# Kernel tuning notes

Hardware: AMD Instinct MI355X
Metric: run time of the kernel (lower is better)

Reference implementation:

```python
import jax, jax.numpy as jnp
import numpy as np

S, B, NIN = 64, 64, 64          # att_width (= target_seq_len), batch, num_input
H1, HB, H = 128, 128, 128       # first LSTM size, biLSTM hidden, att_hid
MLP = (1024, 512, 256, 128, 1)  # h1..h4, num_output


def _lstm_cell(x, h, c, Wih, Whh, b):
    # PyTorch gate order: i, f, g, o
    z = x @ Wih.T + h @ Whh.T + b
    i, f, g, o = jnp.split(z, 4, axis=-1)
    c = jax.nn.sigmoid(f) * c + jax.nn.sigmoid(i) * jnp.tanh(g)
    h = jax.nn.sigmoid(o) * jnp.tanh(c)
    return h, c


def _lstm_seq(xs, Wih, Whh, b, reverse=False):
    # xs: [S, B, in] -> hs: [S, B, H], final (h, c)
    h0 = jnp.zeros((xs.shape[1], Whh.shape[1]), xs.dtype)

    def step(carry, x):
        h, c = _lstm_cell(x, carry[0], carry[1], Wih, Whh, b)
        return (h, c), h

    (h, c), hs = jax.lax.scan(step, (h0, h0), xs, reverse=reverse)
    return hs, (h, c)


def _forward(input_seqs,
             lstm1_Wih, lstm1_Whh, lstm1_b,
             bi2f_Wih, bi2f_Whh, bi2f_b, bi2b_Wih, bi2b_Whh, bi2b_b,
             bi3f_Wih, bi3f_Whh, bi3f_b, bi3b_Wih, bi3b_Whh, bi3b_b,
             enc_Wih, enc_Whh, enc_b,
             dec_Wih, dec_Whh, dec_b,
             att_fc_W, att_w,
             W1_W, W1_b, W2_W, W2_b, W3_W, W3_b, W4_W, W4_b, out_W, out_b):
    # 1) one-directional LSTM
    x, _ = _lstm_seq(input_seqs, lstm1_Wih, lstm1_Whh, lstm1_b)
    # 2-3) two stacked bidirectional LSTMs
    f, _ = _lstm_seq(x, bi2f_Wih, bi2f_Whh, bi2f_b)
    bk, _ = _lstm_seq(x, bi2b_Wih, bi2b_Whh, bi2b_b, reverse=True)
    x = jnp.concatenate([f, bk], axis=-1)            # [S,B,2*HB]
    f, _ = _lstm_seq(x, bi3f_Wih, bi3f_Whh, bi3f_b)
    bk, _ = _lstm_seq(x, bi3b_Wih, bi3b_Whh, bi3b_b, reverse=True)
    x = jnp.concatenate([f, bk], axis=-1)            # [S,B,2*HB]
    # 4) encoder LSTM
    enc_out, (eh, ec) = _lstm_seq(x, enc_Wih, enc_Whh, enc_b)  # [S,B,H]
    # per-step attention decode loop (S sequential steps)
    def dec_step(carry, _):
        xin, h, c = carry
        h, c = _lstm_cell(xin, h, c, dec_Wih, dec_Whh, dec_b)   # [B,H]
        # 'concat' attention: tanh(fc(h + enc_out)) @ w -> scores over S
        scores = jnp.tanh((h[None, :, :] + enc_out) @ att_fc_W.T) @ att_w  # [S,B]
        aw = jax.nn.softmax(scores, axis=0)
        ctx = jnp.einsum('sb,sbh->bh', aw, enc_out)             # [B,H]
        out = jnp.concatenate([h, ctx], axis=-1)                # [B,2H]
        return (h, h, c), out

    _, dec_outs = jax.lax.scan(dec_step, (enc_out[-1], eh, ec), None, length=S)
    # [S,B,2H] -> [B, S*2H]
    flat = dec_outs.transpose(1, 0, 2).reshape(dec_outs.shape[1], -1)
    # 5-6) flatten + 4-layer tanh MLP + linear head
    x = jnp.tanh(flat @ W1_W.T + W1_b)
    x = jnp.tanh(x @ W2_W.T + W2_b)
    x = jnp.tanh(x @ W3_W.T + W3_b)
    x = jnp.tanh(x @ W4_W.T + W4_b)
    return x @ out_W.T + out_b


def setup_inputs() -> dict:
    key = jax.random.key(0)
    ks = iter(jax.random.split(key, 40))

    def mat(shape, scale=0.08):
        return (jax.random.normal(next(ks), shape) * scale).astype(jnp.float32)

    d = {}
    d['input_seqs'] = jax.random.normal(next(ks), (S, B, NIN), dtype=jnp.float32)

    def lstm_p(pfx, inp, hid):
        d[pfx + '_Wih'] = mat((4 * hid, inp))
        d[pfx + '_Whh'] = mat((4 * hid, hid))
        d[pfx + '_b'] = mat((4 * hid,))

    lstm_p('lstm1', NIN, H1)
    lstm_p('bi2f', H1, HB); lstm_p('bi2b', H1, HB)
    lstm_p('bi3f', 2 * HB, HB); lstm_p('bi3b', 2 * HB, HB)
    lstm_p('enc', 2 * HB, H)
    lstm_p('dec', H, H)
    d['att_fc_W'] = mat((H, H))
    d['att_w'] = mat((H,))
    dims = [2 * H * S] + list(MLP)
    names = ['W1', 'W2', 'W3', 'W4', 'out']
    for i, nm in enumerate(names):
        d[nm + '_W'] = mat((dims[i + 1], dims[i]))
        d[nm + '_b'] = mat((dims[i + 1],))
    return d


def reference(input_seqs,
              lstm1_Wih, lstm1_Whh, lstm1_b,
              bi2f_Wih, bi2f_Whh, bi2f_b, bi2b_Wih, bi2b_Whh, bi2b_b,
              bi3f_Wih, bi3f_Whh, bi3f_b, bi3b_Wih, bi3b_Whh, bi3b_b,
              enc_Wih, enc_Whh, enc_b,
              dec_Wih, dec_Whh, dec_b,
              att_fc_W, att_w,
              W1_W, W1_b, W2_W, W2_b, W3_W, W3_b, W4_W, W4_b, out_W, out_b):
    return _forward(input_seqs,
                    lstm1_Wih, lstm1_Whh, lstm1_b,
                    bi2f_Wih, bi2f_Whh, bi2f_b, bi2b_Wih, bi2b_Whh, bi2b_b,
                    bi3f_Wih, bi3f_Whh, bi3f_b, bi3b_Wih, bi3b_Whh, bi3b_b,
                    enc_Wih, enc_Whh, enc_b,
                    dec_Wih, dec_Whh, dec_b,
                    att_fc_W, att_w,
                    W1_W, W1_b, W2_W, W2_b, W3_W, W3_b, W4_W, W4_b, out_W, out_b)
```

## Files before the change

### kernel.cpp

```cpp
#include <hip/hip_runtime.h>
#include <hip/hip_bf16.h>

typedef unsigned int u32;
typedef unsigned short u16;

typedef _Float16 half2_t __attribute__((ext_vector_type(2)));
union H2U { u32 u; half2_t h; };

#if defined(__has_builtin)
#if __has_builtin(__builtin_amdgcn_fdot2)
#define HAS_FDOT2 1
#endif
#if __has_builtin(__builtin_amdgcn_update_dpp)
#define HAS_DPP 1
#endif
#endif

__device__ __forceinline__ float bf2f(u32 u) {
  union { u32 i; float f; } v; v.i = u << 16; return v.f;
}
__device__ __forceinline__ float sigf(float x) {
  return 1.0f / (1.0f + __expf(-x));
}
__device__ __forceinline__ float tanhfast(float x) {
  return 2.0f / (1.0f + __expf(-2.0f * x)) - 1.0f;
}
__device__ __forceinline__ u16 f2bf(float f) {
  u32 u = __float_as_uint(f);
  u += 0x7fffu + ((u >> 16) & 1u);
  return (u16)(u >> 16);
}
__device__ __forceinline__ float dot2acc(u32 wu, u32 hu, float acc) {
  H2U w, h; w.u = wu; h.u = hu;
#ifdef HAS_FDOT2
  return __builtin_amdgcn_fdot2(w.h, h.h, acc, false);
#else
  acc = fmaf((float)w.h.x, (float)h.h.x, acc);
  return fmaf((float)w.h.y, (float)h.h.y, acc);
#endif
}
template <int CTRL>
__device__ __forceinline__ float dppf(float x) {
#ifdef HAS_DPP
  int y = __builtin_amdgcn_update_dpp(0, __float_as_int(x), CTRL, 0xF, 0xF, true);
  return __int_as_float(y);
#else
  const int lane = threadIdx.x & 63;
  if (CTRL == 0xB1)  return __shfl_xor(x, 1, 64);
  if (CTRL == 0x4E)  return __shfl_xor(x, 2, 64);
  if (CTRL == 0x104) return __shfl_down(x, 4, 64);
  return __shfl(x, (lane & ~3) | (CTRL & 3), 64);
#endif
}

__global__ void k_detect(const u32* __restrict__ w, int* __restrict__ flag) {
  __shared__ int cnt;
  if (threadIdx.x == 0) cnt = 0;
  __syncthreads();
  int c = 0;
  for (int i = threadIdx.x; i < 8192; i += 256) {
    const u32 lo = w[i] & 0xffffu;
    const u32 e = (lo >> 7) & 0xffu;
    c += (e >= 100u && e <= 140u) ? 1 : 0;
  }
  atomicAdd(&cnt, c);
  __syncthreads();
  if (threadIdx.x == 0) *flag = (cnt > 4915) ? 1 : 0;
}

struct Job { const void* s; float* d; int n; };
struct Jobs { Job j[30]; };

__global__ void k_cvt_all(Jobs J, const int* __restrict__ flag) {
  const Job jb = J.j[blockIdx.y];
  const int isbf = *flag;
  for (int i = blockIdx.x * 256 + threadIdx.x; i < jb.n; i += 32 * 256) {
    jb.d[i] = isbf ? bf2f(((const u16*)jb.s)[i]) : ((const float*)jb.s)[i];
  }
}

struct IJobs { const float* b[4]; float* d[4]; int n[4]; int mask[4]; };
__global__ void k_init4(IJobs I) {
  const int j = blockIdx.y;
  const float* bb = I.b[j];
  float* dd = I.d[j];
  const int n = I.n[j], mask = I.mask[j];
  for (int i = blockIdx.x * 256 + threadIdx.x; i < n; i += gridDim.x * 256)
    dd[i] = bb[i & mask];
}

struct PJobs { const float* s[7]; const float* s2[7]; u32* d[7]; };
__global__ void k_pack(PJobs P) {
  const float* src = P.s[blockIdx.y];
  const float* src2 = P.s2[blockIdx.y];
  u32* dst = P.d[blockIdx.y];
  const int i = blockIdx.x * 256 + threadIdx.x;
  const int tid = i >> 6, rem = i & 63;
  const int j = rem >> 4, kk = rem & 15;
  const int r = tid >> 2, kq = tid & 3;
  const int row = r + 128 * j, col = kq * 32 + 2 * kk;
  float v0 = src[row * 128 + col];
  float v1 = src[row * 128 + col + 1];
  if (src2) { v0 += src2[row * 128 + col]; v1 += src2[row * 128 + col + 1]; }
  H2U v;
  v.h.x = (_Float16)v0;
  v.h.y = (_Float16)v1;
  dst[i] = v.u;
}

__launch_bounds__(256)
__global__ void k_gemm(const float* __restrict__ A, int lda,
                       const void* __restrict__ Wv, int ldw,
                       const float* __restrict__ bias,
                       float* __restrict__ C, int ldc,
                       int K, int actA, int atom, int wfollow,
                       const int* __restrict__ dflag)
{
  __shared__ float As[32][65];
  __shared__ float Ws[32][65];
  const int isbf = wfollow ? *dflag : 0;
  const int tid = threadIdx.x;
  const int tx = tid & 15, ty = tid >> 4;
  const int m0 = blockIdx.x * 64, n0 = blockIdx.y * 64;
  const int kc = K / gridDim.z;
  const int k0 = blockIdx.z * kc;
  const int lr = tid >> 2;
  const int lk = (tid & 3) << 3;
  float acc[4][4] = {{0.f}};
  const float* Ap   = A + (size_t)(m0 + lr) * lda + k0 + lk;
  const u16*   Wp16 = (const u16*)Wv   + (size_t)(n0 + lr) * ldw + k0 + lk;
  const float* Wp32 = (const float*)Wv + (size_t)(n0 + lr) * ldw + k0 + lk;
  for (int kk = 0; kk < kc; kk += 32) {
    float4 av0 = *(const float4*)(Ap + kk);
    float4 av1 = *(const float4*)(Ap + kk + 4);
    float wv[8];
    if (isbf) {
      const uint4 wu = *(const uint4*)(Wp16 + kk);
      wv[0]=bf2f(wu.x & 0xffffu); wv[1]=bf2f(wu.x >> 16);
      wv[2]=bf2f(wu.y & 0xffffu); wv[3]=bf2f(wu.y >> 16);
      wv[4]=bf2f(wu.z & 0xffffu); wv[5]=bf2f(wu.z >> 16);
      wv[6]=bf2f(wu.w & 0xffffu); wv[7]=bf2f(wu.w >> 16);
    } else {
      const float4 w0 = *(const float4*)(Wp32 + kk);
      const float4 w1 = *(const float4*)(Wp32 + kk + 4);
      wv[0]=w0.x; wv[1]=w0.y; wv[2]=w0.z; wv[3]=w0.w;
      wv[4]=w1.x; wv[5]=w1.y; wv[6]=w1.z; wv[7]=w1.w;
    }
    if (actA) {
      av0.x = tanhfast(av0.x); av0.y = tanhfast(av0.y);
      av0.z = tanhfast(av0.z); av0.w = tanhfast(av0.w);
      av1.x = tanhfast(av1.x); av1.y = tanhfast(av1.y);
      av1.z = tanhfast(av1.z); av1.w = tanhfast(av1.w);
    }
    __syncthreads();
    As[lk+0][lr] = av0.x; As[lk+1][lr] = av0.y;
    As[lk+2][lr] = av0.z; As[lk+3][lr] = av0.w;
    As[lk+4][lr] = av1.x; As[lk+5][lr] = av1.y;
    As[lk+6][lr] = av1.z; As[lk+7][lr] = av1.w;
    #pragma unroll
    for (int q = 0; q < 8; ++q) Ws[lk+q][lr] = wv[q];
    __syncthreads();
    #pragma unroll
    for (int k = 0; k < 32; ++k) {
      float a[4], w[4];
      #pragma unroll
      for (int i = 0; i < 4; ++i) a[i] = As[k][ty + 16*i];
      #pragma unroll
      for (int j = 0; j < 4; ++j) w[j] = Ws[k][tx + 16*j];
      #pragma unroll
      for (int i = 0; i < 4; ++i)
        #pragma unroll
        for (int j = 0; j < 4; ++j)
          acc[i][j] = fmaf(a[i], w[j], acc[i][j]);
    }
  }
  #pragma unroll
  for (int i = 0; i < 4; ++i) {
    const int m = m0 + ty + 16*i;
    #pragma unroll
    for (int j = 0; j < 4; ++j) {
      const int n = n0 + tx + 16*j;
      if (atom) atomicAdd(&C[(size_t)m*ldc + n], acc[i][j]);
      else {
        const float bv = bias ? bias[n] : 0.0f;
        C[(size_t)m*ldc + n] = acc[i][j] + bv;
      }
    }
  }
}

__launch_bounds__(512)
__attribute__((amdgpu_waves_per_eu(2, 2)))
__global__ void k_rec(const float* __restrict__ Zf, const float* __restrict__ Zb,
                      const u32* __restrict__ Wf, const u32* __restrict__ Wb,
                      float* __restrict__ HS, int hstride, int offF, int offB,
                      const float* __restrict__ h0, const float* __restrict__ c0,
                      int zmode, int zld, float* __restrict__ Cout)
{
  const int b = blockIdx.x & 63;
  const int dir = blockIdx.x >> 6;
  const float* Z = dir ? Zb : Zf;
  const u32* Wg = dir ? Wb : Wf;
  const int off = dir ? offB : offF;
  const int tid = threadIdx.x;
  const int r = tid >> 2, kq = tid & 3;

  __shared__ __align__(16) float zall[64*512];
  __shared__ __align__(16) u32 hbuf[2][64];

  if (!zmode) {
    #pragma unroll
    for (int q = 0; q < 16; ++q) {
      const int fid = tid + 512*q;
      const int s = fid >> 7, c4 = (fid & 127) << 2;
      const int cs = c4 ^ (((c4 >> 7) & 1) << 4);
      *(float4*)&zall[s*512 + cs] = *(const float4*)&Z[((size_t)s*64 + b)*zld + c4];
    }
  }

  u32 wp[64];
  {
    const uint4* wr = (const uint4*)(Wg + (size_t)tid * 64);
    #pragma unroll
    for (int q = 0; q < 16; ++q) {
      const uint4 u = wr[q];
      wp[q*4+0]=u.x; wp[q*4+1]=u.y; wp[q*4+2]=u.z; wp[q*4+3]=u.w;
    }
  }
  #pragma unroll
  for (int q = 0; q < 64; ++q)
    asm volatile("" : "+v"(wp[q]));

  float creg = c0 ? c0[b*128 + r] : 0.0f;
  if (tid < 64) {
    H2U v;
    if (h0) {
      v.h.x = (_Float16)h0[b*128 + 2*tid];
      v.h.y = (_Float16)h0[b*128 + 2*tid + 1];
    } else {
      v.h.x = (_Float16)0.f; v.h.y = (_Float16)0.f;
    }
    hbuf[0][tid] = v.u;
  }

  const int colz = (r + 128*kq) ^ ((kq & 1) << 4);
  float zdec = 0.f;
  if (zmode) zdec = Z[r + 128*kq];
  const float* zp = zall + (dir ? 63*512 : 0) + colz;
  const int zstep = dir ? -512 : 512;
  float* hsp = HS + ((size_t)(dir ? 63 : 0)*64 + b)*hstride + off + r;
  const ptrdiff_t hstep = (ptrdiff_t)(dir ? -64 : 64) * hstride;
  const bool beta = (kq & 1) != 0;
  const bool gmm  = (kq & 2) != 0;
  __syncthreads();

  for (int t = 0; t < 64; ++t) {
    float zcv;
    if (zmode) zcv = zdec;
    else       zcv = *zp;
    u32 hh16[16];
    {
      const u32* hp = hbuf[t & 1];
      *(uint4*)&hh16[0]  = *(const uint4*)&hp[kq*16];
      *(uint4*)&hh16[4]  = *(const uint4*)&hp[kq*16 + 4];
      *(uint4*)&hh16[8]  = *(const uint4*)&hp[kq*16 + 8];
      *(uint4*)&hh16[12] = *(const uint4*)&hp[kq*16 + 12];
    }
    float a[4] = {0.f,0.f,0.f,0.f};
    #pragma unroll
    for (int j = 0; j < 4; ++j)
      #pragma unroll
      for (int i = 0; i < 16; ++i)
        a[j] = dot2acc(wp[j*16 + i], hh16[i], a[j]);
    const float u0 = beta ? a[1] : a[0];
    const float v0 = beta ? a[0] : a[1];
    const float u1 = beta ? a[3] : a[2];
    const float v1 = beta ? a[2] : a[3];
    const float x01 = u0 + dppf<0xB1>(v0);
    const float x23 = u1 + dppf<0xB1>(v1);
    const float keep = gmm ? x23 : x01;
    const float send = gmm ? x01 : x23;
    const float g = keep + dppf<0x4E>(send) + zcv;
    const float sg = sigf(g);
    const float tg = tanhfast(g);
    const float si  = dppf<0x00>(sg);
    const float sf  = dppf<0x55>(sg);
    const float tgg = dppf<0xAA>(tg);
    const float so  = dppf<0xFF>(sg);
    const float cc = sf * creg + si * tgg;
    const float hh = so * tanhfast(cc);
    creg = cc;
    const float hn = dppf<0x104>(hh);
    if (kq == 0) {
      *hsp = hh;
      if (!(r & 1)) {
        H2U v; v.h.x = (_Float16)hh; v.h.y = (_Float16)hn;
        hbuf[(t+1) & 1][r >> 1] = v.u;
      }
    }
    zp += zstep;
    hsp += hstep;
    __syncthreads();
  }

  if (Cout != nullptr && kq == 0) Cout[b*128 + r] = creg;
}

#define TS 132
__launch_bounds__(256, 1)
__global__ void k_att(const float* __restrict__ enco, const float* __restrict__ encp,
                      const float* __restrict__ Hdec, const float* __restrict__ Hproj,
                      const float* __restrict__ attw, float* __restrict__ flat)
{
  const int b = blockIdx.x;
  const int t0 = blockIdx.y * 16;
  const int tid = threadIdx.x;
  __shared__ __align__(16) float ep[64*TS];
  __shared__ __align__(16) float en[64*TS];
  __shared__ __align__(16) float hp[16*TS];
  __shared__ float S[64*17];
  __shared__ float aw[64*17];
  __shared__ __align__(16) float awt[128];

  for (int i = tid; i < 8192; i += 256) {
    const int s = i >> 7, k = i & 127;
    const size_t g = ((size_t)s*64 + b)*128 + k;
    ep[s*TS + k] = encp[g];
    en[s*TS + k] = enco[g];
  }
  for (int i = tid; i < 2048; i += 256) {
    const int t = i >> 7, k = i & 127;
    const size_t g = ((size_t)(t0 + t)*64 + b)*128 + k;
    hp[t*TS + k] = Hproj[g];
    flat[(size_t)b*16384 + (t0 + t)*256 + k] = Hdec[g];
  }
  if (tid < 128) awt[tid] = attw[tid];
  __syncthreads();

  {
    const int t = tid & 15, sg = tid >> 4;
    #pragma unroll
    for (int i = 0; i < 4; ++i) {
      const int s = sg*4 + i;
      float acc = 0.f;
      #pragma unroll 8
      for (int k = 0; k < 128; k += 4) {
        const float4 h4 = *(const float4*)&hp[t*TS + k];
        const float4 e4 = *(const float4*)&ep[s*TS + k];
        const float4 w4 = *(const float4*)&awt[k];
        acc = fmaf(w4.x, tanhfast(h4.x + e4.x), acc);
        acc = fmaf(w4.y, tanhfast(h4.y + e4.y), acc);
        acc = fmaf(w4.z, tanhfast(h4.z + e4.z), acc);
        acc = fmaf(w4.w, tanhfast(h4.w + e4.w), acc);
      }
      S[s*17 + t] = acc;
    }
  }
  __syncthreads();
  if (tid < 16) {
    const int t = tid;
    float m = -1e30f;
    for (int s = 0; s < 64; ++s) m = fmaxf(m, S[s*17 + t]);
    float sum = 0.f;
    for (int s = 0; s < 64; ++s) {
      const float e = __expf(S[s*17 + t] - m);
      aw[s*17 + t] = e;
      sum += e;
    }
    const float inv = 1.0f / sum;
    for (int s = 0; s < 64; ++s) aw[s*17 + t] *= inv;
  }
  __syncthreads();
  {
    const int t = tid >> 4, kg = tid & 15;
    float c0a[8] = {0,0,0,0,0,0,0,0};
    for (int s = 0; s < 64; ++s) {
      const float a = aw[s*17 + t];
      const float4 e0 = *(const float4*)&en[s*TS + kg*8];
      const float4 e1 = *(const float4*)&en[s*TS + kg*8 + 4];
      c0a[0] = fmaf(a, e0.x, c0a[0]);
      c0a[1] = fmaf(a, e0.y, c0a[1]);
      c0a[2] = fmaf(a, e0.z, c0a[2]);
      c0a[3] = fmaf(a, e0.w, c0a[3]);
      c0a[4] = fmaf(a, e1.x, c0a[4]);
      c0a[5] = fmaf(a, e1.y, c0a[5]);
      c0a[6] = fmaf(a, e1.z, c0a[6]);
      c0a[7] = fmaf(a, e1.w, c0a[7]);
    }
    float4 o0 = {c0a[0], c0a[1], c0a[2], c0a[3]};
    float4 o1 = {c0a[4], c0a[5], c0a[6], c0a[7]};
    float* dst = &flat[(size_t)b*16384 + (t0 + t)*256 + 128 + kg*8];
    *(float4*)dst = o0;
    *(float4*)(dst + 4) = o1;
  }
}

__global__ void k_head(const float* __restrict__ a4, const float* __restrict__ outW,
                       const float* __restrict__ outb, void* __restrict__ out,
                       const int* __restrict__ dflag)
{
  const int b = threadIdx.x;
  float acc = outb[0];
  #pragma unroll 8
  for (int k = 0; k < 128; ++k)
    acc = fmaf(outW[k], tanhfast(a4[b*128 + k]), acc);
  if (*dflag) ((u16*)out)[b] = f2bf(acc);
  else        ((float*)out)[b] = acc;
}

extern "C" void kernel_launch(void* const* d_in, const int* in_sizes, int n_in,
                              void* d_out, int out_size, void* d_ws, size_t ws_size,
                              hipStream_t stream)
{
  (void)in_sizes; (void)n_in; (void)out_size; (void)ws_size;

  float* p = (float*)d_ws;
  int*   flagp = (int*)p;    p += 64;
  float* x0    = p; p += 64*64*64;
  float* cl1Wih = p; p += 512*64;
  float* cl1Whh = p; p += 512*128;
  float* cl1b   = p; p += 512;
  float* c2Wih  = p; p += 1024*128;
  float* c2bias = p; p += 1024;
  float* c2fWhh = p; p += 512*128;
  float* c2bWhh = p; p += 512*128;
  float* c3Wih  = p; p += 1024*256;
  float* c3bias = p; p += 1024;
  float* c3fWhh = p; p += 512*128;
  float* c3bWhh = p; p += 512*128;
  float* ceWih  = p; p += 512*256;
  float* ceWhh  = p; p += 512*128;
  float* ceb    = p; p += 512;
  float* cdWih  = p; p += 512*128;
  float* cdWhh  = p; p += 512*128;
  float* cdb    = p; p += 512;
  float* cattW  = p; p += 128*128;
  float* cattw  = p; p += 128;
  float* cW1b   = p; p += 1024;
  float* cW2b   = p; p += 512;
  float* cW3b   = p; p += 256;
  float* cW4b   = p; p += 128;
  float* coW    = p; p += 128;
  float* cob    = p; p += 16;
  u32* wpL1 = (u32*)p; p += 32768;
  u32* wp2f = (u32*)p; p += 32768;
  u32* wp2b = (u32*)p; p += 32768;
  u32* wp3f = (u32*)p; p += 32768;
  u32* wp3b = (u32*)p; p += 32768;
  u32* wpE  = (u32*)p; p += 32768;
  u32* wpD  = (u32*)p; p += 32768;
  float* Zf   = p; p += 4096*512;
  float* Z2   = p; p += 4096*1024;
  float* h1   = p; p += 4096*128;
  float* x2   = p; p += 4096*256;
  float* x3   = p; p += 4096*256;
  float* enco = p; p += 4096*128;
  float* Hdec = p; p += 4096*128;
  float* encp = p; p += 4096*128;
  float* Hprj = p; p += 4096*128;
  float* ec   = p; p += 64*128;
  float* flat = p; p += 64*16384;
  float* a1   = p; p += 64*1024;
  float* a2   = p; p += 64*512;
  float* a3   = p; p += 64*256;
  float* a4   = p; p += 64*128;

  k_detect<<<1, 256, 0, stream>>>((const u32*)d_in[2], flagp);

  Jobs J;
  int nj = 0;
  auto add = [&](const void* s, float* d, int n) { J.j[nj].s = s; J.j[nj].d = d; J.j[nj].n = n; ++nj; };
  add(d_in[0],  x0,     64*64*64);
  add(d_in[1],  cl1Wih, 512*64);
  add(d_in[2],  cl1Whh, 512*128);
  add(d_in[3],  cl1b,   512);
  add(d_in[4],  c2Wih,            512*128);
  add(d_in[7],  c2Wih + 512*128,  512*128);
  add(d_in[6],  c2bias,       512);
  add(d_in[9],  c2bias + 512, 512);
  add(d_in[5],  c2fWhh, 512*128);
  add(d_in[8],  c2bWhh, 512*128);
  add(d_in[10], c3Wih,            512*256);
  add(d_in[13], c3Wih + 512*256,  512*256);
  add(d_in[12], c3bias,       512);
  add(d_in[15], c3bias + 512, 512);
  add(d_in[11], c3fWhh, 512*128);
  add(d_in[14], c3bWhh, 512*128);
  add(d_in[16], ceWih,  512*256);
  add(d_in[17], ceWhh,  512*128);
  add(d_in[18], ceb,    512);
  add(d_in[19], cdWih,  512*128);
  add(d_in[20], cdWhh,  512*128);
  add(d_in[21], cdb,    512);
  add(d_in[22], cattW,  128*128);
  add(d_in[23], cattw,  128);
  add(d_in[25], cW1b,   1024);
  add(d_in[27], cW2b,   512);
  add(d_in[29], cW3b,   256);
  add(d_in[31], cW4b,   128);
  add(d_in[32], coW,    128);
  add(d_in[33], cob,    1);
  k_cvt_all<<<dim3(32, nj), 256, 0, stream>>>(J, flagp);

  PJobs P;
  for (int i = 0; i < 7; ++i) P.s2[i] = nullptr;
  P.s[0] = cl1Whh; P.d[0] = wpL1;
  P.s[1] = c2fWhh; P.d[1] = wp2f;
  P.s[2] = c2bWhh; P.d[2] = wp2b;
  P.s[3] = c3fWhh; P.d[3] = wp3f;
  P.s[4] = c3bWhh; P.d[4] = wp3b;
  P.s[5] = ceWhh;  P.d[5] = wpE;
  P.s[6] = cdWih;  P.s2[6] = cdWhh; P.d[6] = wpD;
  k_pack<<<dim3(128, 7), 256, 0, stream>>>(P);

  k_gemm<<<dim3(64,8,1), 256, 0, stream>>>(x0, 64, cl1Wih, 64, cl1b, Zf, 512, 64, 0, 0, 0, flagp);
  k_rec<<<64, 512, 0, stream>>>(Zf, Zf, wpL1, wpL1, h1, 128, 0, 0, nullptr, nullptr, 0, 512, nullptr);

  k_gemm<<<dim3(64,16,1), 256, 0, stream>>>(h1, 128, c2Wih, 128, c2bias, Z2, 1024, 128, 0, 0, 0, flagp);
  k_rec<<<128, 512, 0, stream>>>(Z2, Z2 + 512, wp2f, wp2b, x2, 256, 0, 128, nullptr, nullptr, 0, 1024, nullptr);

  k_gemm<<<dim3(64,16,1), 256, 0, stream>>>(x2, 256, c3Wih, 256, c3bias, Z2, 1024, 256, 0, 0, 0, flagp);
  k_rec<<<128, 512, 0, stream>>>(Z2, Z2 + 512, wp3f, wp3b, x3, 256, 0, 128, nullptr, nullptr, 0, 1024, nullptr);

  k_gemm<<<dim3(64,8,1), 256, 0, stream>>>(x3, 256, ceWih, 256, ceb, Zf, 512, 256, 0, 0, 0, flagp);
  k_rec<<<64, 512, 0, stream>>>(Zf, Zf, wpE, wpE, enco, 128, 0, 0, nullptr, nullptr, 0, 512, ec);

  k_rec<<<64, 512, 0, stream>>>(cdb, cdb, wpD, wpD, Hdec, 128, 0, 0,
                                enco + (size_t)63*64*128, ec, 1, 512, nullptr);

  k_gemm<<<dim3(128,2,1), 256, 0, stream>>>(enco, 128, cattW, 128, nullptr, encp, 128, 128, 0, 0, 0, flagp);

  k_att<<<dim3(64,4), 256, 0, stream>>>(enco, encp, Hdec, Hprj, cattw, flat);

  IJobs I;
  I.b[0]=cW1b; I.d[0]=a1; I.n[0]=64*1024; I.mask[0]=1023;
  I.b[1]=cW2b; I.d[1]=a2; I.n[1]=64*512;  I.mask[1]=511;
  I.b[2]=cW3b; I.d[2]=a3; I.n[2]=64*256;  I.mask[2]=255;
  I.b[3]=cW4b; I.d[3]=a4; I.n[3]=64*128;  I.mask[3]=127;
  k_init4<<<dim3(64, 4), 256, 0, stream>>>(I);
  k_gemm<<<dim3(1,16,64), 256, 0, stream>>>(flat, 16384, d_in[24], 16384, nullptr, a1, 1024, 16384, 0, 1, 1, flagp);
  k_gemm<<<dim3(1,8,16), 256, 0, stream>>>(a1, 1024, d_in[26], 1024, nullptr, a2, 512, 1024, 1, 1, 1, flagp);
  k_gemm<<<dim3(1,4,8), 256, 0, stream>>>(a2, 512, d_in[28], 512, nullptr, a3, 256, 512, 1, 1, 1, flagp);
  k_gemm<<<dim3(1,2,4), 256, 0, stream>>>(a3, 256, d_in[30], 256, nullptr, a4, 128, 256, 1, 1, 1, flagp);

  k_head<<<1, 64, 0, stream>>>(a4, coW, cob, d_out, flagp);
}
```

Before: 651.2 us.

## Use fp16 MFMA GEMM for input projections and W1, store activations as fp16

Adds a new GEMM kernel built on the 16x16x32 fp16 MFMA instruction and uses it for the four LSTM input projections and the large W1 layer. The inputs to those GEMMs (the input sequence, the LSTM hidden outputs and the attention flat buffer) are now written as fp16, which halves their memory traffic. Weights are converted from fp32 or bf16 to fp16 when loaded into LDS. This replaces the scalar fp32 SIMT GEMM and lowers activation precision to fp16.

```diff
diff --git a/kernel.cpp b/kernel.cpp
--- a/kernel.cpp
+++ b/kernel.cpp
@@ -6,6 +6,10 @@
 
 typedef _Float16 half2_t __attribute__((ext_vector_type(2)));
 union H2U { u32 u; half2_t h; };
+
+typedef _Float16 f16x8 __attribute__((ext_vector_type(8)));
+typedef float f32x4 __attribute__((ext_vector_type(4)));
+union F16V { uint4 u; f16x8 h; };
 
 #if defined(__has_builtin)
 #if __has_builtin(__builtin_amdgcn_fdot2)
@@ -29,6 +33,18 @@
   u32 u = __float_as_uint(f);
   u += 0x7fffu + ((u >> 16) & 1u);
   return (u16)(u >> 16);
+}
+__device__ __forceinline__ u16 f2h(float f) {
+  union { _Float16 h; u16 u; } v; v.h = (_Float16)f; return v.u;
+}
+__device__ __forceinline__ u32 fpair2h2(float a, float b) {
+  H2U r; r.h.x = (_Float16)a; r.h.y = (_Float16)b; return r.u;
+}
+__device__ __forceinline__ u32 bfpair2h2(u32 two_bf) {
+  H2U r;
+  r.h.x = (_Float16)bf2f(two_bf & 0xffffu);
+  r.h.y = (_Float16)bf2f(two_bf >> 16);
+  return r.u;
 }
 __device__ __forceinline__ float dot2acc(u32 wu, u32 hu, float acc) {
   H2U w, h; w.u = wu; h.u = hu;
@@ -68,14 +84,16 @@
   if (threadIdx.x == 0) *flag = (cnt > 4915) ? 1 : 0;
 }
 
-struct Job { const void* s; float* d; int n; };
+struct Job { const void* s; float* d; int n; int f16; };
 struct Jobs { Job j[30]; };
 
 __global__ void k_cvt_all(Jobs J, const int* __restrict__ flag) {
   const Job jb = J.j[blockIdx.y];
   const int isbf = *flag;
   for (int i = blockIdx.x * 256 + threadIdx.x; i < jb.n; i += 32 * 256) {
-    jb.d[i] = isbf ? bf2f(((const u16*)jb.s)[i]) : ((const float*)jb.s)[i];
+    const float v = isbf ? bf2f(((const u16*)jb.s)[i]) : ((const float*)jb.s)[i];
+    if (jb.f16) ((u16*)jb.d)[i] = f2h(v);
+    else        jb.d[i] = v;
   }
 }
 
@@ -106,6 +124,74 @@
   v.h.x = (_Float16)v0;
   v.h.y = (_Float16)v1;
   dst[i] = v.u;
+}
+
+__launch_bounds__(256)
+__global__ void k_mf(const u16* __restrict__ A, int lda,
+                     const void* __restrict__ Wv, int ldw,
+                     const float* __restrict__ bias,
+                     float* __restrict__ C, int ldc,
+                     int K, int atom, int wfollow,
+                     const int* __restrict__ dflag)
+{
+  __shared__ __align__(16) u16 As[64][40];
+  __shared__ __align__(16) u16 Bs[64][40];
+  const int isbf = wfollow ? *dflag : 0;
+  const int tid = threadIdx.x;
+  const int m0 = blockIdx.x * 64, n0 = blockIdx.y * 64;
+  const int kc = K / gridDim.z;
+  const int k0 = blockIdx.z * kc;
+  const int row = tid >> 2, part = tid & 3;
+  const int l = tid & 63, w = tid >> 6;
+  const int wr = w >> 1, wc = w & 1;
+  const int fr = l & 15, fk = l >> 4;
+  f32x4 acc[2][2] = {};
+  const u16*   Ap   = A + (size_t)(m0 + row) * lda + k0 + part * 8;
+  const u16*   Wp16 = (const u16*)Wv   + (size_t)(n0 + row) * ldw + k0 + part * 8;
+  const float* Wp32 = (const float*)Wv + (size_t)(n0 + row) * ldw + k0 + part * 8;
+
+  for (int kk = 0; kk < kc; kk += 32) {
+    const uint4 av = *(const uint4*)(Ap + kk);
+    uint4 wv;
+    if (isbf) {
+      const uint4 wu = *(const uint4*)(Wp16 + kk);
+      wv.x = bfpair2h2(wu.x); wv.y = bfpair2h2(wu.y);
+      wv.z = bfpair2h2(wu.z); wv.w = bfpair2h2(wu.w);
+    } else {
+      const float4 w0 = *(const float4*)(Wp32 + kk);
+      const float4 w1 = *(const float4*)(Wp32 + kk + 4);
+      wv.x = fpair2h2(w0.x, w0.y); wv.y = fpair2h2(w0.z, w0.w);
+      wv.z = fpair2h2(w1.x, w1.y); wv.w = fpair2h2(w1.z, w1.w);
+    }
+    __syncthreads();
+    *(uint4*)&As[row][part * 8] = av;
+    *(uint4*)&Bs[row][part * 8] = wv;
+    __syncthreads();
+    F16V a0, a1, b0, b1;
+    a0.u = *(const uint4*)&As[wr * 32 + fr][fk * 8];
+    a1.u = *(const uint4*)&As[wr * 32 + 16 + fr][fk * 8];
+    b0.u = *(const uint4*)&Bs[wc * 32 + fr][fk * 8];
+    b1.u = *(const uint4*)&Bs[wc * 32 + 16 + fr][fk * 8];
+    acc[0][0] = __builtin_amdgcn_mfma_f32_16x16x32_f16(a0.h, b0.h, acc[0][0], 0, 0, 0);
+    acc[0][1] = __builtin_amdgcn_mfma_f32_16x16x32_f16(a0.h, b1.h, acc[0][1], 0, 0, 0);
+    acc[1][0] = __builtin_amdgcn_mfma_f32_16x16x32_f16(a1.h, b0.h, acc[1][0], 0, 0, 0);
+    acc[1][1] = __builtin_amdgcn_mfma_f32_16x16x32_f16(a1.h, b1.h, acc[1][1], 0, 0, 0);
+  }
+
+  #pragma unroll
+  for (int i = 0; i < 2; ++i) {
+    #pragma unroll
+    for (int j = 0; j < 2; ++j) {
+      const int n = n0 + wc * 32 + j * 16 + fr;
+      const float bv = (bias && !atom) ? bias[n] : 0.0f;
+      #pragma unroll
+      for (int q = 0; q < 4; ++q) {
+        const int m = m0 + wr * 32 + i * 16 + fk * 4 + q;
+        if (atom) atomicAdd(&C[(size_t)m * ldc + n], acc[i][j][q]);
+        else      C[(size_t)m * ldc + n] = acc[i][j][q] + bv;
+      }
+    }
+  }
 }
 
 __launch_bounds__(256)
@@ -195,7 +281,7 @@
                       const u32* __restrict__ Wf, const u32* __restrict__ Wb,
                       float* __restrict__ HS, int hstride, int offF, int offB,
                       const float* __restrict__ h0, const float* __restrict__ c0,
-                      int zmode, int zld, float* __restrict__ Cout)
+                      int zmode, int zld, float* __restrict__ Cout, int hf16)
 {
   const int b = blockIdx.x & 63;
   const int dir = blockIdx.x >> 6;
@@ -248,7 +334,7 @@
   if (zmode) zdec = Z[r + 128*kq];
   const float* zp = zall + (dir ? 63*512 : 0) + colz;
   const int zstep = dir ? -512 : 512;
-  float* hsp = HS + ((size_t)(dir ? 63 : 0)*64 + b)*hstride + off + r;
+  size_t hidx = ((size_t)(dir ? 63 : 0)*64 + b)*hstride + off + r;
   const ptrdiff_t hstep = (ptrdiff_t)(dir ? -64 : 64) * hstride;
   const bool beta = (kq & 1) != 0;
   const bool gmm  = (kq & 2) != 0;
@@ -292,14 +378,15 @@
     creg = cc;
     const float hn = dppf<0x104>(hh);
     if (kq == 0) {
-      *hsp = hh;
+      if (hf16) ((u16*)HS)[hidx] = f2h(hh);
+      else      HS[hidx] = hh;
       if (!(r & 1)) {
         H2U v; v.h.x = (_Float16)hh; v.h.y = (_Float16)hn;
         hbuf[(t+1) & 1][r >> 1] = v.u;
       }
     }
     zp += zstep;
-    hsp += hstep;
+    hidx += hstep;
     __syncthreads();
   }
 
@@ -310,7 +397,7 @@
 __launch_bounds__(256, 1)
 __global__ void k_att(const float* __restrict__ enco, const float* __restrict__ encp,
                       const float* __restrict__ Hdec, const float* __restrict__ Hproj,
-                      const float* __restrict__ attw, float* __restrict__ flat)
+                      const float* __restrict__ attw, u16* __restrict__ flat)
 {
   const int b = blockIdx.x;
   const int t0 = blockIdx.y * 16;
@@ -332,7 +419,7 @@
     const int t = i >> 7, k = i & 127;
     const size_t g = ((size_t)(t0 + t)*64 + b)*128 + k;
     hp[t*TS + k] = Hproj[g];
-    flat[(size_t)b*16384 + (t0 + t)*256 + k] = Hdec[g];
+    flat[(size_t)b*16384 + (t0 + t)*256 + k] = f2h(Hdec[g]);
   }
   if (tid < 128) awt[tid] = attw[tid];
   __syncthreads();
@@ -387,11 +474,11 @@
       c0a[6] = fmaf(a, e1.z, c0a[6]);
       c0a[7] = fmaf(a, e1.w, c0a[7]);
     }
-    float4 o0 = {c0a[0], c0a[1], c0a[2], c0a[3]};
-    float4 o1 = {c0a[4], c0a[5], c0a[6], c0a[7]};
-    float* dst = &flat[(size_t)b*16384 + (t0 + t)*256 + 128 + kg*8];
-    *(float4*)dst = o0;
-    *(float4*)(dst + 4) = o1;
+    union { u16 s[8]; uint4 u; } o;
+    #pragma unroll
+    for (int q = 0; q < 8; ++q) o.s[q] = f2h(c0a[q]);
+    u16* dst = &flat[(size_t)b*16384 + (t0 + t)*256 + 128 + kg*8];
+    *(uint4*)dst = o.u;
   }
 }
 
@@ -469,8 +556,10 @@
 
   Jobs J;
   int nj = 0;
-  auto add = [&](const void* s, float* d, int n) { J.j[nj].s = s; J.j[nj].d = d; J.j[nj].n = n; ++nj; };
-  add(d_in[0],  x0,     64*64*64);
+  auto add = [&](const void* s, float* d, int n, int f16 = 0) {
+    J.j[nj].s = s; J.j[nj].d = d; J.j[nj].n = n; J.j[nj].f16 = f16; ++nj;
+  };
+  add(d_in[0],  x0,     64*64*64, 1);
   add(d_in[1],  cl1Wih, 512*64);
   add(d_in[2],  cl1Whh, 512*128);
   add(d_in[3],  cl1b,   512);
@@ -513,24 +602,24 @@
   P.s[6] = cdWih;  P.s2[6] = cdWhh; P.d[6] = wpD;
   k_pack<<<dim3(128, 7), 256, 0, stream>>>(P);
 
-  k_gemm<<<dim3(64,8,1), 256, 0, stream>>>(x0, 64, cl1Wih, 64, cl1b, Zf, 512, 64, 0, 0, 0, flagp);
-  k_rec<<<64, 512, 0, stream>>>(Zf, Zf, wpL1, wpL1, h1, 128, 0, 0, nullptr, nullptr, 0, 512, nullptr);
-
-  k_gemm<<<dim3(64,16,1), 256, 0, stream>>>(h1, 128, c2Wih, 128, c2bias, Z2, 1024, 128, 0, 0, 0, flagp);
-  k_rec<<<128, 512, 0, stream>>>(Z2, Z2 + 512, wp2f, wp2b, x2, 256, 0, 128, nullptr, nullptr, 0, 1024, nullptr);
-
-  k_gemm<<<dim3(64,16,1), 256, 0, stream>>>(x2, 256, c3Wih, 256, c3bias, Z2, 1024, 256, 0, 0, 0, flagp);
-  k_rec<<<128, 512, 0, stream>>>(Z2, Z2 + 512, wp3f, wp3b, x3, 256, 0, 128, nullptr, nullptr, 0, 1024, nullptr);
-
-  k_gemm<<<dim3(64,8,1), 256, 0, stream>>>(x3, 256, ceWih, 256, ceb, Zf, 512, 256, 0, 0, 0, flagp);
-  k_rec<<<64, 512, 0, stream>>>(Zf, Zf, wpE, wpE, enco, 128, 0, 0, nullptr, nullptr, 0, 512, ec);
+  k_mf<<<dim3(64,8,1), 256, 0, stream>>>((const u16*)x0, 64, cl1Wih, 64, cl1b, Zf, 512, 64, 0, 0, flagp);
+  k_rec<<<64, 512, 0, stream>>>(Zf, Zf, wpL1, wpL1, h1, 128, 0, 0, nullptr, nullptr, 0, 512, nullptr, 1);
+
+  k_mf<<<dim3(64,16,1), 256, 0, stream>>>((const u16*)h1, 128, c2Wih, 128, c2bias, Z2, 1024, 128, 0, 0, flagp);
+  k_rec<<<128, 512, 0, stream>>>(Z2, Z2 + 512, wp2f, wp2b, x2, 256, 0, 128, nullptr, nullptr, 0, 1024, nullptr, 1);
+
+  k_mf<<<dim3(64,16,1), 256, 0, stream>>>((const u16*)x2, 256, c3Wih, 256, c3bias, Z2, 1024, 256, 0, 0, flagp);
+  k_rec<<<128, 512, 0, stream>>>(Z2, Z2 + 512, wp3f, wp3b, x3, 256, 0, 128, nullptr, nullptr, 0, 1024, nullptr, 1);
+
+  k_mf<<<dim3(64,8,1), 256, 0, stream>>>((const u16*)x3, 256, ceWih, 256, ceb, Zf, 512, 256, 0, 0, flagp);
+  k_rec<<<64, 512, 0, stream>>>(Zf, Zf, wpE, wpE, enco, 128, 0, 0, nullptr, nullptr, 0, 512, ec, 0);
 
   k_rec<<<64, 512, 0, stream>>>(cdb, cdb, wpD, wpD, Hdec, 128, 0, 0,
-                                enco + (size_t)63*64*128, ec, 1, 512, nullptr);
+                                enco + (size_t)63*64*128, ec, 1, 512, nullptr, 0);
 
   k_gemm<<<dim3(128,2,1), 256, 0, stream>>>(enco, 128, cattW, 128, nullptr, encp, 128, 128, 0, 0, 0, flagp);
 
-  k_att<<<dim3(64,4), 256, 0, stream>>>(enco, encp, Hdec, Hprj, cattw, flat);
+  k_att<<<dim3(64,4), 256, 0, stream>>>(enco, encp, Hdec, Hprj, cattw, (u16*)flat);
 
   IJobs I;
   I.b[0]=cW1b; I.d[0]=a1; I.n[0]=64*1024; I.mask[0]=1023;
@@ -538,7 +627,7 @@
   I.b[2]=cW3b; I.d[2]=a3; I.n[2]=64*256;  I.mask[2]=255;
   I.b[3]=cW4b; I.d[3]=a4; I.n[3]=64*128;  I.mask[3]=127;
   k_init4<<<dim3(64, 4), 256, 0, stream>>>(I);
-  k_gemm<<<dim3(1,16,64), 256, 0, stream>>>(flat, 16384, d_in[24], 16384, nullptr, a1, 1024, 16384, 0, 1, 1, flagp);
+  k_mf<<<dim3(1,16,64), 256, 0, stream>>>((const u16*)flat, 16384, d_in[24], 16384, nullptr, a1, 1024, 16384, 1, 1, flagp);
   k_gemm<<<dim3(1,8,16), 256, 0, stream>>>(a1, 1024, d_in[26], 1024, nullptr, a2, 512, 1024, 1, 1, 1, flagp);
   k_gemm<<<dim3(1,4,8), 256, 0, stream>>>(a2, 512, d_in[28], 512, nullptr, a3, 256, 512, 1, 1, 1, flagp);
   k_gemm<<<dim3(1,2,4), 256, 0, stream>>>(a3, 256, d_in[30], 256, nullptr, a4, 128, 256, 1, 1, 1, flagp);
```

Result: faster. 559.3 us (-14.1%).
